# Performance work log

Measured on AMD Instinct MI355X. Metric: run time of the kernel, lower is better.

The kernel has to match this reference:

```python
import jax, jax.numpy as jnp
import numpy as np

# ---- dims (see shape_source) ----
N, EG, T = 10000, 120000, 600000
NR, NS = 16, 7                      # num_radial, num_spherical
EA, EE, ET, ERBF, ECBF, EBIL = 128, 256, 64, 16, 16, 64
NB = 2                              # num_blocks
CUTOFF = 6.0
MAXZ = 100
INV_SQRT2 = 0.7071067811865476


def scaled_silu(x):
    # GemNet 'swish' activation = ScaledSiLU
    return jax.nn.silu(x) * (1.0 / 0.6)


def layer_norm(x, w, b):
    mu = jnp.mean(x, -1, keepdims=True)
    v = jnp.var(x, -1, keepdims=True)
    return (x - mu) * jax.lax.rsqrt(v + 1e-5) * w + b


def radial_basis(D):
    # polynomial envelope (exponent 5) * gaussian RBF on d/cutoff
    d = D / CUTOFF
    p = 5.0
    env = 1.0 - ((p + 1) * (p + 2) / 2) * d**5 + p * (p + 2) * d**6 - (p * (p + 1) / 2) * d**7
    env = jnp.where(d < 1.0, env, 0.0)
    offsets = jnp.linspace(0.0, 1.0, NR)
    coeff = -0.5 * (NR - 1.0) ** 2   # -0.5 / spacing^2
    return env[:, None] * jnp.exp(coeff * (d[:, None] - offsets) ** 2)  # (EG, NR)


def spherical_basis(cosphi):
    # circular basis: Y_l0(phi) = sqrt((2l+1)/4pi) P_l(cos phi), l = 0..NS-1
    P = [jnp.ones_like(cosphi), cosphi]
    for l in range(2, NS):
        P.append(((2 * l - 1) * cosphi * P[-1] - (l - 1) * P[-2]) / l)
    return jnp.stack([np.sqrt((2 * l + 1) / (4 * np.pi)) * P[l] for l in range(NS)], -1)  # (T, NS)


def residual(x, Ws):
    # GemNet ResidualLayer: 2 bias-free dense + skip, scaled by 1/sqrt(2)
    y = scaled_silu(scaled_silu(x @ Ws[0]) @ Ws[1])
    return (x + y) * INV_SQRT2


def gemnet_forward(D, cosphi, atom_emb, W_rbf3, W_rbf_h, W_rbf_out, W_cbf_down,
                   W_edge_emb, ib_dense_ca, ib_trip_dense_ba, ib_trip_mlp_rbf,
                   ib_trip_down, ib_trip_bilinear, ib_trip_up_ca, ib_trip_up_ac,
                   ib_res_before, ib_res_after, ib_atom_dense_rbf, ib_atom_dense1,
                   ib_atom_res, ib_concat_dense, ib_res_m, ob_dense_rbf, ob_dense1,
                   ob_res, ln_m_w, ln_m_b, ln_E_w, ln_E_b,
                   Z, idx_s, idx_t, id3_ba, id3_ca, id_swap):
    rbf = radial_basis(D)                                   # (EG, NR)
    sph = spherical_basis(cosphi)                           # (T, NS)
    rbf3 = rbf @ W_rbf3                                     # (EG, ERBF)
    rbf_h = rbf @ W_rbf_h
    rbf_out = rbf @ W_rbf_out
    # EfficientInteractionDownProjection: rbf x W -> (EG, NS, ECBF)
    rbf_W1 = jnp.einsum('er,sri->esi', rbf, W_cbf_down)
    # per-triplet circular-basis embedding: sum over spherical components
    cbf_t = jnp.einsum('ts,tsi->ti', sph, rbf_W1[id3_ca])   # (T, ECBF)

    h = atom_emb[Z]                                         # (N, EA)
    m = scaled_silu(jnp.concatenate([h[idx_s], h[idx_t], rbf], -1) @ W_edge_emb)  # (EG, EE)

    def out_block(i, h_cur, m_cur):
        mn = layer_norm(m_cur, ln_m_w[i], ln_m_b[i])
        x = mn * (rbf_out @ ob_dense_rbf[i])                # (EG, EE)
        xE = jax.ops.segment_sum(x, idx_t, num_segments=N)  # scatter edges -> atoms
        xE = scaled_silu(xE @ ob_dense1[i])                 # (N, EA)
        for r in range(ob_res.shape[1]):
            xE = residual(xE, ob_res[i, r])
        return layer_norm(xE, ln_E_w[i], ln_E_b[i])

    E_t = out_block(0, h, m)
    for i in range(NB):
        # ---- triplet interaction ----
        x_ca_skip = scaled_silu(m @ ib_dense_ca[i])
        x_ba = scaled_silu(m @ ib_trip_dense_ba[i])
        x_ba = x_ba * (rbf3 @ ib_trip_mlp_rbf[i])
        x_trip = scaled_silu(x_ba @ ib_trip_down[i])        # (EG, ET)
        x_t = x_trip[id3_ba]                                # gather -> (T, ET)
        # bilinear: out[t,o] = sum_i cbf_t[t,i] * sum_c x_t[t,c] W[c,i,o]
        Wb = ib_trip_bilinear[i]                            # (ET, ECBF, EBIL)
        acc = (x_t @ Wb[:, 0, :]) * cbf_t[:, 0:1]
        for ic in range(1, ECBF):
            acc = acc + (x_t @ Wb[:, ic, :]) * cbf_t[:, ic:ic + 1]
        x = jax.ops.segment_sum(acc, id3_ca, num_segments=EG)  # scatter trip -> edges (EG, EBIL)
        x_ca = scaled_silu(x @ ib_trip_up_ca[i])
        x_ac = scaled_silu(x @ ib_trip_up_ac[i])[id_swap]   # counter-directional edge
        x3 = (x_ca + x_ac) * INV_SQRT2

        # ---- edge update ----
        x = (x_ca_skip + x3) * INV_SQRT2
        for r in range(ib_res_before.shape[1]):
            x = residual(x, ib_res_before[i, r])
        x = (x + m) * INV_SQRT2
        for r in range(ib_res_after.shape[1]):
            x = residual(x, ib_res_after[i, r])

        # ---- atom update ----
        xa = x * (rbf_h @ ib_atom_dense_rbf[i])
        xa = jax.ops.segment_sum(xa, idx_t, num_segments=N)
        xa = scaled_silu(xa @ ib_atom_dense1[i])            # (N, EA)
        for r in range(ib_atom_res.shape[1]):
            xa = residual(xa, ib_atom_res[i, r])
        h = (h + xa) * INV_SQRT2

        # ---- edge embedding refresh with updated atoms ----
        m2 = scaled_silu(jnp.concatenate([h[idx_s], h[idx_t], x], -1) @ ib_concat_dense[i])
        for r in range(ib_res_m.shape[1]):
            m2 = residual(m2, ib_res_m[i, r])
        m = (m + m2) * INV_SQRT2

        E_t = E_t + out_block(i + 1, h, m)
    return E_t  # (N, EA) per-atom output features


def setup_inputs() -> dict:
    key = jax.random.key(0)
    ks = iter(jax.random.split(key, 64))

    def nrm(shape, fan_in):
        return jax.random.normal(next(ks), shape, jnp.float32) / np.sqrt(fan_in)

    Z = jax.random.randint(next(ks), (N,), 0, MAXZ)
    idx_s = jax.random.randint(next(ks), (EG,), 0, N)
    idx_t = jax.random.randint(next(ks), (EG,), 0, N)
    id3_ba = jax.random.randint(next(ks), (T,), 0, EG)
    id3_ca = jax.random.randint(next(ks), (T,), 0, EG)
    id_swap = jnp.arange(EG) ^ 1   # symmetric edges stored in (e, e^1) pairs
    D = jax.random.uniform(next(ks), (EG,), jnp.float32, 0.8, 5.9)
    cosphi = jax.random.uniform(next(ks), (T,), jnp.float32, -1.0, 1.0)

    emb = jax.random.normal(next(ks), (MAXZ, EA), jnp.float32)
    emb = emb / jnp.maximum(jnp.linalg.norm(emb, axis=-1, keepdims=True), 1.0)  # max_norm=1

    NBo = NB + 1
    inp = dict(
        D=D, cosphi=cosphi, atom_emb=emb,
        W_rbf3=nrm((NR, ERBF), NR), W_rbf_h=nrm((NR, ERBF), NR), W_rbf_out=nrm((NR, ERBF), NR),
        W_cbf_down=nrm((NS, NR, ECBF), NR),
        W_edge_emb=nrm((2 * EA + NR, EE), 2 * EA + NR),
        ib_dense_ca=nrm((NB, EE, EE), EE),
        ib_trip_dense_ba=nrm((NB, EE, EE), EE),
        ib_trip_mlp_rbf=nrm((NB, ERBF, EE), ERBF),
        ib_trip_down=nrm((NB, EE, ET), EE),
        ib_trip_bilinear=nrm((NB, ET, ECBF, EBIL), ET * ECBF),
        ib_trip_up_ca=nrm((NB, EBIL, EE), EBIL),
        ib_trip_up_ac=nrm((NB, EBIL, EE), EBIL),
        ib_res_before=nrm((NB, 1, 2, EE, EE), EE),
        ib_res_after=nrm((NB, 1, 2, EE, EE), EE),
        ib_atom_dense_rbf=nrm((NB, ERBF, EE), ERBF),
        ib_atom_dense1=nrm((NB, EE, EA), EE),
        ib_atom_res=nrm((NB, 2, 2, EA, EA), EA),
        ib_concat_dense=nrm((NB, 2 * EA + EE, EE), 2 * EA + EE),
        ib_res_m=nrm((NB, 1, 2, EE, EE), EE),
        ob_dense_rbf=nrm((NBo, ERBF, EE), ERBF),
        ob_dense1=nrm((NBo, EE, EA), EE),
        ob_res=nrm((NBo, 2, 2, EA, EA), EA),
        ln_m_w=jnp.ones((NBo, EE)), ln_m_b=jnp.zeros((NBo, EE)),
        ln_E_w=jnp.ones((NBo, EA)), ln_E_b=jnp.zeros((NBo, EA)),
        Z=Z, idx_s=idx_s, idx_t=idx_t, id3_ba=id3_ba, id3_ca=id3_ca, id_swap=id_swap,
    )
    return inp


def reference(D, cosphi, atom_emb, W_rbf3, W_rbf_h, W_rbf_out, W_cbf_down, W_edge_emb,
              ib_dense_ca, ib_trip_dense_ba, ib_trip_mlp_rbf, ib_trip_down,
              ib_trip_bilinear, ib_trip_up_ca, ib_trip_up_ac, ib_res_before,
              ib_res_after, ib_atom_dense_rbf, ib_atom_dense1, ib_atom_res,
              ib_concat_dense, ib_res_m, ob_dense_rbf, ob_dense1, ob_res,
              ln_m_w, ln_m_b, ln_E_w, ln_E_b, Z, idx_s, idx_t, id3_ba, id3_ca, id_swap):
    return gemnet_forward(D, cosphi, atom_emb, W_rbf3, W_rbf_h, W_rbf_out, W_cbf_down,
                          W_edge_emb, ib_dense_ca, ib_trip_dense_ba, ib_trip_mlp_rbf,
                          ib_trip_down, ib_trip_bilinear, ib_trip_up_ca, ib_trip_up_ac,
                          ib_res_before, ib_res_after, ib_atom_dense_rbf, ib_atom_dense1,
                          ib_atom_res, ib_concat_dense, ib_res_m, ob_dense_rbf, ob_dense1,
                          ob_res, ln_m_w, ln_m_b, ln_E_w, ln_E_b,
                          Z, idx_s, idx_t, id3_ba, id3_ca, id_swap)
```

## Files before the change

### kernel.cpp

```cpp
#include <hip/hip_runtime.h>

#define NATOM 10000
#define EG    120000
#define TT    600000

#define INV_SQRT2f 0.7071067811865476f

typedef unsigned short bf16t;
typedef __attribute__((ext_vector_type(8))) short s16x8;
typedef __attribute__((ext_vector_type(8))) unsigned short u16x8;
typedef __attribute__((ext_vector_type(4))) float f32x4;

__device__ __forceinline__ float ssilu(float x) {
    return x * (1.0f / (1.0f + __expf(-x))) * (1.0f / 0.6f);
}
__device__ __forceinline__ float bf2f(unsigned short u) {
    return __uint_as_float(((unsigned)u) << 16);
}
__device__ __forceinline__ unsigned short f2bf(float f) {
    unsigned b = __float_as_uint(f);
    unsigned r = (b + 0x7FFF + ((b >> 16) & 1)) >> 16;
    return (unsigned short)r;
}
__device__ __forceinline__ u16x8 cvt8(const float4 va, const float4 vb) {
// ... 144 lines not shown
        r[i] = env * __expf(-112.5f * t * t);
    }
#pragma unroll
    for (int j = 0; j < 16; j++) rbf[(size_t)e * 16 + j] = f2bf(r[j]);
    for (int s = 0; s < 7; s++) {
#pragma unroll 4
        for (int i = 0; i < 16; i++) {
            float a = 0.f;
#pragma unroll
            for (int k = 0; k < 16; k++)
                a = fmaf(r[k], sW[(s * 16 + k) * 16 + i], a);
            rbfW1[(size_t)e * 112 + s * 16 + i] = a;
        }
    }
}

__global__ __launch_bounds__(256) void k_cbf(
    const float* __restrict__ cosphi, const int* __restrict__ id3_ca,
    const float* __restrict__ rbfW1, const int* __restrict__ rank,
    bf16t* __restrict__ cbf)
{
    int t = blockIdx.x * 256 + threadIdx.x;
    if (t >= TT) return;
    float c = cosphi[t];
    const float norm[7] = {0.28209479177387814f, 0.4886025119029199f, 0.6307831305050401f,
                           0.7463526651802308f, 0.8462843753216345f, 0.935414346693485f,
                           1.0171072362820548f};
    float y[7];
    float pm2 = 1.0f, pm1 = c;
    y[0] = norm[0];
    y[1] = norm[1] * c;
    for (int l = 2; l < 7; l++) {
        float p = ((2.0f * l - 1.0f) * c * pm1 - (l - 1.0f) * pm2) / (float)l;
        y[l] = norm[l] * p;
        pm2 = pm1; pm1 = p;
    }
    int e = id3_ca[t];
    const float* __restrict__ w = rbfW1 + (size_t)e * 112;
    float out[16];
#pragma unroll
    for (int i = 0; i < 16; i++) out[i] = 0.f;
#pragma unroll
    for (int s = 0; s < 7; s++) {
        float ys = y[s];
#pragma unroll
        for (int i = 0; i < 16; i++) out[i] = fmaf(ys, w[s * 16 + i], out[i]);
    }
    int p = rank[t];
#pragma unroll
    for (int i = 0; i < 16; i++) cbf[(size_t)p * 16 + i] = f2bf(out[i]);
}

__global__ __launch_bounds__(256) void k_hgather(
    const float* __restrict__ emb, const int* __restrict__ Z, bf16t* __restrict__ h)
{
    int i = blockIdx.x * 256 + threadIdx.x;
    if (i < NATOM * 128) {
        int n = i >> 7, j = i & 127;
        h[i] = f2bf(emb[(size_t)Z[n] * 128 + j]);
    }
}

template <typename TA, int FR, int FC, int EPI>
__global__ __launch_bounds__(256) void mgemm3(
    const TA* __restrict__ A, const bf16t* __restrict__ BT,
    bf16t* __restrict__ C, const bf16t* __restrict__ skip,
    int M, int N, int K)
{
    constexpr int ROWS = 2 * FR * 16;
    constexpr int COLS = 2 * FC * 16;
    __shared__ __align__(16) ushort As[ROWS][40];
    __shared__ __align__(16) ushort Bs[COLS][40];
    const int tid = threadIdx.x, wave = tid >> 6, lane = tid & 63;
    const int waveR = wave >> 1, waveC = wave & 1;
    const int rowBase = blockIdx.y * ROWS, colBase = blockIdx.x * COLS;

    const int sar = tid >> 1, sak = (tid & 1) << 4;
    int agr = rowBase + sar; if (agr >= M) agr = M - 1;
    int sbc, sbk;
    if constexpr (COLS == 128) { sbc = tid >> 1; sbk = (tid & 1) << 4; }
    else                       { sbc = tid >> 2; sbk = (tid & 3) << 3; }

    f32x4 zv = {0.f, 0.f, 0.f, 0.f};
    f32x4 acc[FR][FC];
#pragma unroll
    for (int f = 0; f < FR; f++)
#pragma unroll
        for (int q = 0; q < FC; q++) acc[f][q] = zv;

    const int arow0 = waveR * FR * 16 + (lane & 15);
    const int bcol0 = waveC * FC * 16 + (lane & 15);
    const int kd = (lane >> 4) << 3;

    u16x8 a0, a1, b0, b1;
    auto loadA = [&](int k0) {
        if constexpr (sizeof(TA) == 2) {
            const u16x8* s = (const u16x8*)((const bf16t*)A + (size_t)agr * K + k0 + sak);
            a0 = s[0]; a1 = s[1];
        } else {
            const float4* s = (const float4*)((const float*)A + (size_t)agr * K + k0 + sak);
            a0 = cvt8(s[0], s[1]); a1 = cvt8(s[2], s[3]);
        }
    };
    auto loadB = [&](int k0) {
        const u16x8* s = (const u16x8*)(BT + (size_t)(colBase + sbc) * K + k0 + sbk);
        b0 = s[0];
        if constexpr (COLS == 128) b1 = s[1];
    };
    loadA(0); loadB(0);
    for (int k0 = 0; k0 < K; k0 += 32) {
        __syncthreads();
        *(u16x8*)&As[sar][sak] = a0;
        *(u16x8*)&As[sar][sak + 8] = a1;
        *(u16x8*)&Bs[sbc][sbk] = b0;
        if constexpr (COLS == 128) *(u16x8*)&Bs[sbc][sbk + 8] = b1;
        __syncthreads();
        if (k0 + 32 < K) { loadA(k0 + 32); loadB(k0 + 32); }
        u16x8 af[FR], bf[FC];
#pragma unroll
        for (int f = 0; f < FR; f++) af[f] = *(const u16x8*)&As[arow0 + f * 16][kd];
#pragma unroll
        for (int q = 0; q < FC; q++) bf[q] = *(const u16x8*)&Bs[bcol0 + q * 16][kd];
#pragma unroll
        for (int f = 0; f < FR; f++)
#pragma unroll
            for (int q = 0; q < FC; q++)
                acc[f][q] = __builtin_amdgcn_mfma_f32_16x16x32_bf16(
                    *(s16x8*)&af[f], *(s16x8*)&bf[q], acc[f][q], 0, 0, 0);
    }

    const int rB = rowBase + waveR * FR * 16 + ((lane >> 4) << 2);
    const int cB = colBase + waveC * FC * 16 + (lane & 15);
#pragma unroll
    for (int f = 0; f < FR; f++) {
#pragma unroll
        for (int r = 0; r < 4; r++) {
            int row = rB + f * 16 + r;
            if (row >= M) continue;
#pragma unroll
            for (int q = 0; q < FC; q++) {
                int col = cB + q * 16;
                float v = acc[f][q][r];
                if (EPI == 1) {
                    C[(size_t)row * N + col] = f2bf(ssilu(v));
                } else {
                    float sk = bf2f(skip[(size_t)row * N + col]);
                    C[(size_t)row * N + col] = f2bf((sk + ssilu(v)) * INV_SQRT2f);
                }
            }
        }
    }
}

template <int FCC, int EPIOUT>
__global__ __launch_bounds__(256) void mgemm_res(
    const bf16t* __restrict__ A, const bf16t* __restrict__ BT0,
    const bf16t* __restrict__ BT1, bf16t* __restrict__ C,
    const bf16t* __restrict__ add2, int M)
{
    constexpr int N = FCC * 32;
    __shared__ __align__(16) ushort As[64][40];
    __shared__ __align__(16) ushort Bs[N][40];
    __shared__ __align__(16) ushort inter[64][N + 8];
    const int tid = threadIdx.x, wave = tid >> 6, lane = tid & 63;
    const int waveR = wave >> 1, waveC = wave & 1;
    const int rowBase = blockIdx.x * 64;

    const int sar = tid >> 2, sak = (tid & 3) << 3;
    int agr = rowBase + sar; if (agr >= M) agr = M - 1;
    const int sbc = tid >> 2, sbk = (tid & 3) << 3;

    const int arow0 = waveR * 32 + (lane & 15);
    const int bcol0 = waveC * FCC * 16 + (lane & 15);
    const int kd = (lane >> 4) << 3;

    f32x4 zv = {0.f, 0.f, 0.f, 0.f};
    f32x4 acc[2][FCC];
#pragma unroll
    for (int f = 0; f < 2; f++)
#pragma unroll
        for (int q = 0; q < FCC; q++) acc[f][q] = zv;

    u16x8 aR, bR[FCC / 2];
    auto loadA = [&](int k0) {
        aR = *(const u16x8*)(A + (size_t)agr * N + k0 + sak);
    };
    auto loadB = [&](const bf16t* BT, int k0) {
#pragma unroll
        for (int j = 0; j < FCC / 2; j++)
            bR[j] = *(const u16x8*)(BT + (size_t)(sbc + j * 64) * N + k0 + sbk);
    };

    loadA(0); loadB(BT0, 0);
    for (int k0 = 0; k0 < N; k0 += 32) {
        __syncthreads();
        *(u16x8*)&As[sar][sak] = aR;
#pragma unroll
        for (int j = 0; j < FCC / 2; j++) *(u16x8*)&Bs[sbc + j * 64][sbk] = bR[j];
        __syncthreads();
        if (k0 + 32 < N) { loadA(k0 + 32); loadB(BT0, k0 + 32); }
        else             { loadB(BT1, 0); }
        u16x8 af0 = *(const u16x8*)&As[arow0][kd];
        u16x8 af1 = *(const u16x8*)&As[arow0 + 16][kd];
        u16x8 bf[FCC];
#pragma unroll
        for (int q = 0; q < FCC; q++) bf[q] = *(const u16x8*)&Bs[bcol0 + q * 16][kd];
#pragma unroll
        for (int q = 0; q < FCC; q++) {
            acc[0][q] = __builtin_amdgcn_mfma_f32_16x16x32_bf16(
                *(s16x8*)&af0, *(s16x8*)&bf[q], acc[0][q], 0, 0, 0);
            acc[1][q] = __builtin_amdgcn_mfma_f32_16x16x32_bf16(
                *(s16x8*)&af1, *(s16x8*)&bf[q], acc[1][q], 0, 0, 0);
        }
    }
    {
        const int rL = waveR * 32 + ((lane >> 4) << 2);
        const int cL = waveC * FCC * 16 + (lane & 15);
#pragma unroll
        for (int f = 0; f < 2; f++)
#pragma unroll
            for (int r = 0; r < 4; r++)
#pragma unroll
                for (int q = 0; q < FCC; q++)
                    inter[rL + f * 16 + r][cL + q * 16] = f2bf(ssilu(acc[f][q][r]));
    }
#pragma unroll
    for (int f = 0; f < 2; f++)
#pragma unroll
        for (int q = 0; q < FCC; q++) acc[f][q] = zv;

    for (int k0 = 0; k0 < N; k0 += 32) {
        __syncthreads();
#pragma unroll
        for (int j = 0; j < FCC / 2; j++) *(u16x8*)&Bs[sbc + j * 64][sbk] = bR[j];
        __syncthreads();
        if (k0 + 32 < N) loadB(BT1, k0 + 32);
        u16x8 af0 = *(const u16x8*)&inter[arow0][k0 + kd];
        u16x8 af1 = *(const u16x8*)&inter[arow0 + 16][k0 + kd];
        u16x8 bf[FCC];
#pragma unroll
        for (int q = 0; q < FCC; q++) bf[q] = *(const u16x8*)&Bs[bcol0 + q * 16][kd];
#pragma unroll
        for (int q = 0; q < FCC; q++) {
            acc[0][q] = __builtin_amdgcn_mfma_f32_16x16x32_bf16(
                *(s16x8*)&af0, *(s16x8*)&bf[q], acc[0][q], 0, 0, 0);
            acc[1][q] = __builtin_amdgcn_mfma_f32_16x16x32_bf16(
                *(s16x8*)&af1, *(s16x8*)&bf[q], acc[1][q], 0, 0, 0);
        }
    }

    const int rB = rowBase + waveR * 32 + ((lane >> 4) << 2);
    const int cB = waveC * FCC * 16 + (lane & 15);
#pragma unroll
    for (int f = 0; f < 2; f++) {
#pragma unroll
        for (int r = 0; r < 4; r++) {
            int row = rB + f * 16 + r;
            if (row >= M) continue;
#pragma unroll
            for (int q = 0; q < FCC; q++) {
                int col = cB + q * 16;
                float sk = bf2f(A[(size_t)row * N + col]);
                float y = (sk + ssilu(acc[f][q][r])) * INV_SQRT2f;
                if (EPIOUT == 1) y = (y + bf2f(add2[(size_t)row * N + col])) * INV_SQRT2f;
                C[(size_t)row * N + col] = f2bf(y);
            }
        }
    }
}

__global__ __launch_bounds__(256) void mgemmA1(
    const bf16t* __restrict__ BT, bf16t* __restrict__ C,
    int M, int N, int K, int KP,
    const bf16t* __restrict__ hA, const int* __restrict__ gS,
    const int* __restrict__ gT, const bf16t* __restrict__ X, int w2)
{
    __shared__ __align__(16) ushort As[128][40];
    __shared__ __align__(16) ushort Bs[64][40];
    const int tid = threadIdx.x, wave = tid >> 6, lane = tid & 63;
    const int waveR = wave >> 1, waveC = wave & 1;
    const int rowBase = blockIdx.y * 128, colBase = blockIdx.x * 64;

    const int sar = tid >> 1, sak = (tid & 1) << 4;
    const int arow = rowBase + sar;
    const int arowC = arow < M ? arow : (M - 1);
    const int ia = gS[arowC], ibx = gT[arowC];
    const int sbc = tid >> 2, sbk = (tid & 3) << 3;

    f32x4 zv = {0.f, 0.f, 0.f, 0.f};
    f32x4 acc[4][2];
#pragma unroll
    for (int f = 0; f < 4; f++)
#pragma unroll
        for (int q = 0; q < 2; q++) acc[f][q] = zv;

    const int arow0 = waveR * 64 + (lane & 15);
    const int bcol0 = waveC * 32 + (lane & 15);
    const int kd = (lane >> 4) << 3;

    u16x8 a0, a1, b0;
    auto loadA = [&](int k0) {
        a0 = u16x8{}; a1 = u16x8{};
        const int kk = k0 + sak;
        if (kk < 128) {
            const u16x8* s = (const u16x8*)(hA + (size_t)ia * 128 + kk);
            a0 = s[0]; a1 = s[1];
        } else if (kk < 256) {
            const u16x8* s = (const u16x8*)(hA + (size_t)ibx * 128 + (kk - 128));
            a0 = s[0]; a1 = s[1];
        } else if (kk < K && kk - 256 < w2) {
            const u16x8* s = (const u16x8*)(X + (size_t)arowC * w2 + (kk - 256));
            a0 = s[0]; a1 = s[1];
        }
    };
    auto loadB = [&](int k0) {
        b0 = *(const u16x8*)(BT + (size_t)(colBase + sbc) * KP + k0 + sbk);
    };
    loadA(0); loadB(0);
    for (int k0 = 0; k0 < K; k0 += 32) {
        __syncthreads();
        *(u16x8*)&As[sar][sak] = a0;
        *(u16x8*)&As[sar][sak + 8] = a1;
        *(u16x8*)&Bs[sbc][sbk] = b0;
        __syncthreads();
        if (k0 + 32 < K) { loadA(k0 + 32); loadB(k0 + 32); }
        u16x8 af[4], bf[2];
#pragma unroll
        for (int f = 0; f < 4; f++) af[f] = *(const u16x8*)&As[arow0 + f * 16][kd];
#pragma unroll
        for (int q = 0; q < 2; q++) bf[q] = *(const u16x8*)&Bs[bcol0 + q * 16][kd];
#pragma unroll
        for (int f = 0; f < 4; f++)
#pragma unroll
            for (int q = 0; q < 2; q++)
                acc[f][q] = __builtin_amdgcn_mfma_f32_16x16x32_bf16(
                    *(s16x8*)&af[f], *(s16x8*)&bf[q], acc[f][q], 0, 0, 0);
    }

    const int rB = rowBase + waveR * 64 + ((lane >> 4) << 2);
    const int cB = colBase + waveC * 32 + (lane & 15);
#pragma unroll
    for (int f = 0; f < 4; f++) {
#pragma unroll
        for (int r = 0; r < 4; r++) {
            int row = rB + f * 16 + r;
            if (row >= M) continue;
#pragma unroll
            for (int q = 0; q < 2; q++)
                C[(size_t)row * N + cB + q * 16] = f2bf(ssilu(acc[f][q][r]));
        }
    }
}

__global__ __launch_bounds__(256) void mgemm_up(
    const float* __restrict__ A, const bf16t* __restrict__ BTca,
    const bf16t* __restrict__ BTac, bf16t* __restrict__ C,
    const bf16t* __restrict__ skip, int M)
{
    constexpr int K = 64, N = 256;
    __shared__ __align__(16) ushort As[128][40];
    __shared__ __align__(16) ushort Bs[2][64][40];
    const int tid = threadIdx.x, wave = tid >> 6, lane = tid & 63;
    const int waveR = wave >> 1, waveC = wave & 1;
    const int rowBase = blockIdx.y * 128, colBase = blockIdx.x * 64;

    const int sar = tid >> 1, sak = (tid & 1) << 4;
    int agr = rowBase + sar; if (agr >= M) agr = M - 1;
    const int sbc = tid >> 2, sbk = (tid & 3) << 3;

    f32x4 zv = {0.f, 0.f, 0.f, 0.f};
    f32x4 accA[4][2], accB[4][2];
#pragma unroll
    for (int f = 0; f < 4; f++)
#pragma unroll
        for (int q = 0; q < 2; q++) { accA[f][q] = zv; accB[f][q] = zv; }

    const int arow0 = waveR * 64 + (lane & 15);
    const int bcol0 = waveC * 32 + (lane & 15);
    const int kd = (lane >> 4) << 3;

    u16x8 a0, a1, bA, bB;
    auto loadA = [&](int k0) {
        const float4* s = (const float4*)(A + (size_t)agr * K + k0 + sak);
        a0 = cvt8(s[0], s[1]); a1 = cvt8(s[2], s[3]);
    };
    auto loadB = [&](int k0) {
        bA = *(const u16x8*)(BTca + (size_t)(colBase + sbc) * K + k0 + sbk);
        bB = *(const u16x8*)(BTac + (size_t)(colBase + sbc) * K + k0 + sbk);
    };
    loadA(0); loadB(0);
    for (int k0 = 0; k0 < K; k0 += 32) {
        __syncthreads();
        *(u16x8*)&As[sar][sak] = a0;
        *(u16x8*)&As[sar][sak + 8] = a1;
        *(u16x8*)&Bs[0][sbc][sbk] = bA;
        *(u16x8*)&Bs[1][sbc][sbk] = bB;
        __syncthreads();
        if (k0 + 32 < K) { loadA(k0 + 32); loadB(k0 + 32); }
        u16x8 af[4], bfA[2], bfB[2];
#pragma unroll
        for (int f = 0; f < 4; f++) af[f] = *(const u16x8*)&As[arow0 + f * 16][kd];
#pragma unroll
        for (int q = 0; q < 2; q++) {
            bfA[q] = *(const u16x8*)&Bs[0][bcol0 + q * 16][kd];
            bfB[q] = *(const u16x8*)&Bs[1][bcol0 + q * 16][kd];
        }
#pragma unroll
        for (int f = 0; f < 4; f++)
#pragma unroll
            for (int q = 0; q < 2; q++) {
                accA[f][q] = __builtin_amdgcn_mfma_f32_16x16x32_bf16(
                    *(s16x8*)&af[f], *(s16x8*)&bfA[q], accA[f][q], 0, 0, 0);
                accB[f][q] = __builtin_amdgcn_mfma_f32_16x16x32_bf16(
                    *(s16x8*)&af[f], *(s16x8*)&bfB[q], accB[f][q], 0, 0, 0);
            }
    }

    const int rB = rowBase + waveR * 64 + ((lane >> 4) << 2);
    const int cB = colBase + waveC * 32 + (lane & 15);
#pragma unroll
    for (int f = 0; f < 4; f++) {
#pragma unroll
        for (int r = 0; r < 4; r++) {
            int row = rB + f * 16 + r;
            if (row >= M) continue;
#pragma unroll
            for (int q = 0; q < 2; q++) {
                int col = cB + q * 16;
                float v = (ssilu(accA[f][q][r]) + ssilu(accB[f][q][r ^ 1])) * INV_SQRT2f;
                float y = (bf2f(skip[(size_t)row * N + col]) + v) * INV_SQRT2f;
                C[(size_t)row * N + col] = f2bf(y);
            }
        }
    }
}

__global__ __launch_bounds__(256) void k_bilinear_m(
    const bf16t* __restrict__ xtrip, const bf16t* __restrict__ cbf,
    const bf16t* __restrict__ WT,
    const int* __restrict__ ba_s, const int* __restrict__ ca_s,
    float* __restrict__ seg)
{
    __shared__ __align__(16) ushort xs[64][72];
    __shared__ ushort cbs[64][16];
    __shared__ int cas[64];
    __shared__ __align__(16) ushort ws[2][4096];
    __shared__ __align__(16) float ts[64][65];
    const int tid = threadIdx.x, wave = tid >> 6, lane = tid & 63;
    const int t0 = blockIdx.x * 64;
    {
        int r = tid >> 2, q = (tid & 3) << 4;
        int ba = ba_s[t0 + r];
        const u16x8* src = (const u16x8*)(xtrip + (size_t)ba * 64 + q);
        *(u16x8*)&xs[r][q] = src[0];
        *(u16x8*)&xs[r][q + 8] = src[1];
    }
    if (tid < 64) cas[tid] = ca_s[t0 + tid];
    {
        int e = tid << 2; int r = e >> 4, c = e & 15;
        *(ushort4*)&cbs[r][c] = *(const ushort4*)(cbf + (size_t)(t0 + r) * 16 + c);
    }
    u16x8 g0, g1;
    {
        const u16x8* s = (const u16x8*)(WT + (size_t)tid * 16);
        *(u16x8*)&ws[0][tid * 16] = s[0];
        *(u16x8*)&ws[0][tid * 16 + 8] = s[1];
        const u16x8* s1 = (const u16x8*)(WT + 4096 + (size_t)tid * 16);
        g0 = s1[0]; g1 = s1[1];
    }
    __syncthreads();
    const int kd = (lane >> 4) << 3;
    u16x8 a0 = *(const u16x8*)(&xs[wave * 16 + (lane & 15)][kd]);
    u16x8 a1 = *(const u16x8*)(&xs[wave * 16 + (lane & 15)][32 + kd]);
    const int rowo = wave * 16 + ((lane >> 4) << 2);
    const int chb = lane >> 4, colw = lane & 15;

    float tot[4][4];
#pragma unroll
    for (int a = 0; a < 4; a++)
#pragma unroll
        for (int b = 0; b < 4; b++) tot[a][b] = 0.f;

    for (int i = 0; i < 16; i++) {
        const int cur = i & 1;
        if (i < 15) {
            *(u16x8*)&ws[cur ^ 1][tid * 16] = g0;
            *(u16x8*)&ws[cur ^ 1][tid * 16 + 8] = g1;
        }
        const ushort* wb = ws[cur];
        f32x4 zv = {0.f, 0.f, 0.f, 0.f};
        f32x4 p[4] = {zv, zv, zv, zv};
#pragma unroll
        for (int fc = 0; fc < 4; fc++) {
            u16x8 b0 = *(const u16x8*)&wb[((chb * 64) + colw + fc * 16) * 8];
            u16x8 b1 = *(const u16x8*)&wb[(((4 + chb) * 64) + colw + fc * 16) * 8];
            p[fc] = __builtin_amdgcn_mfma_f32_16x16x32_bf16(
                *(s16x8*)&a0, *(s16x8*)&b0, p[fc], 0, 0, 0);
            p[fc] = __builtin_amdgcn_mfma_f32_16x16x32_bf16(
                *(s16x8*)&a1, *(s16x8*)&b1, p[fc], 0, 0, 0);
        }
#pragma unroll
        for (int r = 0; r < 4; r++) {
            float s = bf2f(cbs[rowo + r][i]);
#pragma unroll
            for (int fc = 0; fc < 4; fc++) tot[fc][r] += s * p[fc][r];
        }
        if (i < 14) {
            const u16x8* s = (const u16x8*)(WT + (size_t)(i + 2) * 4096 + (size_t)tid * 16);
            g0 = s[0]; g1 = s[1];
        }
        __syncthreads();
    }
#pragma unroll
    for (int r = 0; r < 4; r++)
#pragma unroll
        for (int fc = 0; fc < 4; fc++)
            ts[rowo + r][fc * 16 + (lane & 15)] = tot[fc][r];
    __syncthreads();
    {
        int q = tid >> 6, c = tid & 63;
        float s = 0.f;
        int cur = cas[q * 16];
#pragma unroll 1
        for (int r = q * 16; r < q * 16 + 16; r++) {
            int ca = cas[r];
            if (ca != cur) {
                atomicAdd(&seg[(size_t)cur * 64 + c], s);
                s = 0.f; cur = ca;
            }
            s += ts[r][c];
        }
        atomicAdd(&seg[(size_t)cur * 64 + c], s);
    }
}

__global__ __launch_bounds__(256) void k_mulproj(
    const bf16t* __restrict__ in, const bf16t* __restrict__ rvec,
    const float* __restrict__ Wp, bf16t* __restrict__ out)
{
    int e = blockIdx.x;
    int j = threadIdx.x;
    __shared__ float r16[16];
    if (j < 16) r16[j] = bf2f(rvec[(size_t)e * 16 + j]);
    __syncthreads();
    float p = 0.f;
#pragma unroll
    for (int k = 0; k < 16; k++) p = fmaf(r16[k], Wp[k * 256 + j], p);
    out[(size_t)e * 256 + j] = f2bf(bf2f(in[(size_t)e * 256 + j]) * p);
}

__global__ __launch_bounds__(256) void k_ln_proj(
    const bf16t* __restrict__ m, const float* __restrict__ lnw,
    const float* __restrict__ lnb, const bf16t* __restrict__ rvec,
    const float* __restrict__ Wp, bf16t* __restrict__ out)
{
    int e = blockIdx.x;
    int j = threadIdx.x;
    __shared__ float red[8];
    __shared__ float r16[16];
    if (j < 16) r16[j] = bf2f(rvec[(size_t)e * 16 + j]);
    float v = bf2f(m[(size_t)e * 256 + j]);
    float s = v, s2 = v * v;
#pragma unroll
    for (int off = 32; off > 0; off >>= 1) {
        s += __shfl_xor(s, off);
        s2 += __shfl_xor(s2, off);
    }
    int wid = j >> 6, lane = j & 63;
    if (lane == 0) { red[wid] = s; red[4 + wid] = s2; }
    __syncthreads();
    float tot = red[0] + red[1] + red[2] + red[3];
    float tot2 = red[4] + red[5] + red[6] + red[7];
    float mu = tot * (1.f / 256.f);
    float var = tot2 * (1.f / 256.f) - mu * mu;
    float ln = (v - mu) * rsqrtf(var + 1e-5f) * lnw[j] + lnb[j];
    float p = 0.f;
#pragma unroll
    for (int k = 0; k < 16; k++) p = fmaf(r16[k], Wp[k * 256 + j], p);
    out[(size_t)e * 256 + j] = f2bf(ln * p);
}

__global__ __launch_bounds__(128) void k_ln_acc(
    const bf16t* __restrict__ x, const float* __restrict__ w,
    const float* __restrict__ b, float* __restrict__ out)
{
    int n = blockIdx.x;
    int j = threadIdx.x;
    __shared__ float red[4];
    float v = bf2f(x[(size_t)n * 128 + j]);
    float s = v, s2 = v * v;
#pragma unroll
    for (int off = 32; off > 0; off >>= 1) {
        s += __shfl_xor(s, off);
        s2 += __shfl_xor(s2, off);
    }
    int wid = j >> 6, lane = j & 63;
    if (lane == 0) { red[wid] = s; red[2 + wid] = s2; }
    __syncthreads();
    float tot = red[0] + red[1];
    float tot2 = red[2] + red[3];
    float mu = tot * (1.f / 128.f);
    float var = tot2 * (1.f / 128.f) - mu * mu;
    out[(size_t)n * 128 + j] += (v - mu) * rsqrtf(var + 1e-5f) * w[j] + b[j];
}

typedef bf16t T;
static bool try_run(void* const* d_in, void* d_out, void* d_ws, size_t ws_size, hipStream_t stream)
{
    const float* D            = (const float*)d_in[0];
    const float* cosphi       = (const float*)d_in[1];
    const float* atom_emb     = (const float*)d_in[2];
    const float* W_rbf3       = (const float*)d_in[3];
    const float* W_rbf_h      = (const float*)d_in[4];
    const float* W_rbf_out    = (const float*)d_in[5];
    const float* W_cbf_down   = (const float*)d_in[6];
    const float* W_edge_emb   = (const float*)d_in[7];
    const float* ib_dense_ca  = (const float*)d_in[8];
    const float* ib_trip_dense_ba = (const float*)d_in[9];
    const float* ib_trip_mlp_rbf  = (const float*)d_in[10];
    const float* ib_trip_down     = (const float*)d_in[11];
    const float* ib_trip_bilinear = (const float*)d_in[12];
    const float* ib_trip_up_ca    = (const float*)d_in[13];
    const float* ib_trip_up_ac    = (const float*)d_in[14];
    const float* ib_res_before    = (const float*)d_in[15];
    const float* ib_res_after     = (const float*)d_in[16];
    const float* ib_atom_dense_rbf = (const float*)d_in[17];
    const float* ib_atom_dense1    = (const float*)d_in[18];
    const float* ib_atom_res       = (const float*)d_in[19];
    const float* ib_concat_dense   = (const float*)d_in[20];
    const float* ib_res_m          = (const float*)d_in[21];
    const float* ob_dense_rbf      = (const float*)d_in[22];
    const float* ob_dense1         = (const float*)d_in[23];
    const float* ob_res            = (const float*)d_in[24];
    const float* ln_m_w            = (const float*)d_in[25];
    const float* ln_m_b            = (const float*)d_in[26];
    const float* ln_E_w            = (const float*)d_in[27];
    const float* ln_E_b            = (const float*)d_in[28];
    const int* Z       = (const int*)d_in[29];
    const int* idx_s   = (const int*)d_in[30];
    const int* idx_t   = (const int*)d_in[31];
    const int* id3_ba  = (const int*)d_in[32];
    const int* id3_ca  = (const int*)d_in[33];

    char* base = (char*)d_ws;
    size_t off = 0;
    auto alloc = [&](size_t bytes) -> char* {
        off = (off + 255) & ~(size_t)255;
        char* p = base + off;
        off += bytes;
        return p;
    };
    T* m      = (T*)alloc((size_t)EG * 256 * 2);
    T* B1     = (T*)alloc((size_t)EG * 256 * 2);
    T* B2     = (T*)alloc((size_t)EG * 256 * 2);
    float* rbfW1 = (float*)B1;
    int* rank    = (int*)B2;
    T* rbf    = (T*)alloc((size_t)EG * 16 * 2);
    T* cbf    = (T*)alloc((size_t)TT * 16 * 2);
    bf16t* h  = (bf16t*)alloc((size_t)NATOM * 128 * 2);
    T* xtrip  = (T*)alloc((size_t)EG * 64 * 2);
    char* ub  = alloc((size_t)EG * 64 * 4);
    float* seg64  = (float*)ub;
    bf16t* segN_b = (bf16t*)ub;
    bf16t* At1b   = (bf16t*)(ub + (size_t)NATOM * 256 * 2);
    int* cntT  = (int*)ub;
    int* cnt2T = (int*)(ub + (size_t)EG * 4);
    int* off_ca = (int*)(ub + (size_t)2 * EG * 4);
    float* wcb = (float*)alloc((size_t)7 * 4096 * 4);
    bf16t* ar  = (bf16t*)alloc((size_t)507904 * 2);
    int* off_atom  = (int*)alloc((size_t)(NATOM + 1) * 4);
    int* ba_s      = (int*)alloc((size_t)TT * 4);
    int* ca_s      = (int*)alloc((size_t)TT * 4);
    int* csr_edges = (int*)alloc((size_t)EG * 4);
    if (off > ws_size) return false;
    float* out = (float*)d_out;

    auto g256 = [&](const T* A, unsigned wOff, T* C) {
        dim3 grid(2, (EG + 127) / 128);
        mgemm3<T, 4, 4, 1><<<grid, 256, 0, stream>>>(A, ar + wOff, C, nullptr, EG, 256, 256);
    };
    auto gatom1 = [&](const bf16t* A, unsigned wOff, bf16t* C) {
        dim3 grid(1, (NATOM + 127) / 128);
        mgemm3<bf16t, 4, 4, 1><<<grid, 256, 0, stream>>>(A, ar + wOff, C, nullptr, NATOM, 128, 256);
    };
    auto out_block = [&](int i, unsigned offD1, unsigned offRes) {
        k_ln_proj<<<EG, 256, 0, stream>>>(m, ln_m_w + (size_t)i * 256, ln_m_b + (size_t)i * 256,
                                          rbf, wcb + (size_t)(4 + i) * 4096, B2);
        k_segsum<<<NATOM, 256, 0, stream>>>(B2, off_atom, csr_edges, segN_b);
        gatom1(segN_b, offD1, At1b);
        mgemm_res<4, 0><<<(NATOM + 63) / 64, 256, 0, stream>>>(
            At1b, ar + offRes, ar + offRes + 16384, At1b, nullptr, NATOM);
        mgemm_res<4, 0><<<(NATOM + 63) / 64, 256, 0, stream>>>(
            At1b, ar + offRes + 32768, ar + offRes + 49152, At1b, nullptr, NATOM);
        k_ln_acc<<<NATOM, 128, 0, stream>>>(At1b, ln_E_w + (size_t)i * 128, ln_E_b + (size_t)i * 128, out);
    };

    hipMemsetAsync(cntT, 0, (size_t)EG * 4, stream);
    k_hist<<<(TT + 255) / 256, 256, 0, stream>>>(id3_ca, cntT, TT);
    k_scan<<<1, 1024, 0, stream>>>(cntT, off_ca, EG);
    hipMemsetAsync(cnt2T, 0, (size_t)EG * 4, stream);
    k_rank_trip<<<(TT + 255) / 256, 256, 0, stream>>>(id3_ca, id3_ba, off_ca, cnt2T,
                                                      rank, ba_s, ca_s, TT);
    hipMemsetAsync(cntT, 0, (size_t)NATOM * 4, stream);
    k_hist<<<(EG + 255) / 256, 256, 0, stream>>>(idx_t, cntT, EG);
    k_scan<<<1, 1024, 0, stream>>>(cntT, off_atom, NATOM);
    hipMemsetAsync(cnt2T, 0, (size_t)NATOM * 4, stream);
    k_rank_edge<<<(EG + 255) / 256, 256, 0, stream>>>(idx_t, off_atom, cnt2T, csr_edges, EG);

    {
        WcBatch wb;
        wb.e[0] = {W_rbf3, ib_trip_mlp_rbf};
        wb.e[1] = {W_rbf3, ib_trip_mlp_rbf + 4096};
        wb.e[2] = {W_rbf_h, ib_atom_dense_rbf};
        wb.e[3] = {W_rbf_h, ib_atom_dense_rbf + 4096};
        wb.e[4] = {W_rbf_out, ob_dense_rbf};
        wb.e[5] = {W_rbf_out, ob_dense_rbf + 4096};
        wb.e[6] = {W_rbf_out, ob_dense_rbf + 8192};
        k_wcomb_batch<<<7, 256, 0, stream>>>(wb, wcb);
    }
    {
        WtBatch wt{};
        wt.e[0] = {W_edge_emb, 0u, 272, 288, 256, 0};
        wt.e[1] = {ob_dense1, 73728u, 256, 256, 128, 0};
        for (int j = 0; j < 4; j++)
            wt.e[2 + j] = {ob_res + (size_t)j * 16384, 106496u + j * 16384u, 128, 128, 128, 0};
        wt.n = 6;
        k_wt_batch<<<512, 256, 0, stream>>>(wt, ar);
    }

    hipMemsetAsync(out, 0, (size_t)NATOM * 128 * 4, stream);
    k_rbf<<<(EG + 255) / 256, 256, 0, stream>>>(D, W_cbf_down, rbf, rbfW1);
    k_cbf<<<(TT + 255) / 256, 256, 0, stream>>>(cosphi, id3_ca, rbfW1, rank, cbf);
    k_hgather<<<(NATOM * 128 + 255) / 256, 256, 0, stream>>>(atom_emb, Z, h);
    {
        dim3 grid(4, (EG + 127) / 128);
        mgemmA1<<<grid, 256, 0, stream>>>(ar, m, EG, 256, 272, 288, h, idx_s, idx_t, rbf, 16);
    }
    out_block(0, 73728u, 106496u);

    for (int i = 0; i < 2; i++) {
        {
            WtBatch wt{};
            wt.e[0] = {ib_dense_ca + (size_t)i * 65536, 0u, 256, 256, 256, 0};
            wt.e[1] = {ib_trip_dense_ba + (size_t)i * 65536, 65536u, 256, 256, 256, 0};
            wt.e[2] = {ib_trip_down + (size_t)i * 16384, 131072u, 256, 256, 64, 0};
            wt.e[3] = {ib_trip_bilinear + (size_t)i * 65536, 147456u, 0, 0, 0, 1};
            wt.e[4] = {ib_trip_up_ca + (size_t)i * 16384, 212992u, 64, 64, 256, 0};
            wt.e[5] = {ib_trip_up_ac + (size_t)i * 16384, 229376u, 64, 64, 256, 0};
            wt.e[6] = {ib_res_before + (size_t)i * 131072, 245760u, 256, 256, 256, 0};
            wt.e[7] = {ib_res_before + (size_t)i * 131072 + 65536, 311296u, 256, 256, 256, 0};
            wt.e[8] = {ib_res_after + (size_t)i * 131072, 376832u, 256, 256, 256, 0};
            wt.e[9] = {ib_res_after + (size_t)i * 131072 + 65536, 442368u, 256, 256, 256, 0};
            wt.n = 10;
            k_wt_batch<<<512, 256, 0, stream>>>(wt, ar);
        }
        g256(m, 0u, B1);
        g256(m, 65536u, B2);
        k_mulproj<<<EG, 256, 0, stream>>>(B2, rbf, wcb + (size_t)i * 4096, B2);
        {
            dim3 grid(1, (EG + 127) / 128);
            mgemm3<T, 4, 2, 1><<<grid, 256, 0, stream>>>(B2, ar + 131072, xtrip, nullptr, EG, 64, 256);
        }
        hipMemsetAsync(seg64, 0, (size_t)EG * 64 * 4, stream);
        k_bilinear_m<<<TT / 64, 256, 0, stream>>>(xtrip, cbf, ar + 147456, ba_s, ca_s, seg64);
        {
            dim3 grid(4, (EG + 127) / 128);
            mgemm_up<<<grid, 256, 0, stream>>>(seg64, ar + 212992, ar + 229376, B1, B1, EG);
        }
        mgemm_res<8, 1><<<EG / 64, 256, 0, stream>>>(B1, ar + 245760, ar + 311296, B1, m, EG);
        mgemm_res<8, 0><<<EG / 64, 256, 0, stream>>>(B1, ar + 376832, ar + 442368, B1, nullptr, EG);
        {
            WtBatch wt{};
            wt.e[0] = {ib_atom_dense1 + (size_t)i * 32768, 0u, 256, 256, 128, 0};
            for (int j = 0; j < 4; j++)
                wt.e[1 + j] = {ib_atom_res + (size_t)i * 65536 + (size_t)j * 16384,
                               32768u + j * 16384u, 128, 128, 128, 0};
            wt.e[5] = {ib_concat_dense + (size_t)i * 131072, 98304u, 512, 512, 256, 0};
            wt.e[6] = {ib_res_m + (size_t)i * 131072, 229376u, 256, 256, 256, 0};
            wt.e[7] = {ib_res_m + (size_t)i * 131072 + 65536, 294912u, 256, 256, 256, 0};
            wt.e[8] = {ob_dense1 + (size_t)(i + 1) * 32768, 360448u, 256, 256, 128, 0};
            wt.n = 9;
            k_wt_batch<<<512, 256, 0, stream>>>(wt, ar);
            WtBatch wt2{};
            for (int j = 0; j < 4; j++)
                wt2.e[j] = {ob_res + (size_t)(i + 1) * 65536 + (size_t)j * 16384,
                            393216u + j * 16384u, 128, 128, 128, 0};
            wt2.n = 4;
            k_wt_batch<<<512, 256, 0, stream>>>(wt2, ar);
        }
        k_mulproj<<<EG, 256, 0, stream>>>(B1, rbf, wcb + (size_t)(2 + i) * 4096, B2);
        k_segsum<<<NATOM, 256, 0, stream>>>(B2, off_atom, csr_edges, segN_b);
        gatom1(segN_b, 0u, At1b);
        mgemm_res<4, 0><<<(NATOM + 63) / 64, 256, 0, stream>>>(
            At1b, ar + 32768, ar + 49152, At1b, nullptr, NATOM);
        mgemm_res<4, 1><<<(NATOM + 63) / 64, 256, 0, stream>>>(
            At1b, ar + 65536, ar + 81920, h, h, NATOM);
        {
            dim3 grid(4, (EG + 127) / 128);
            mgemmA1<<<grid, 256, 0, stream>>>(ar + 98304, B2, EG, 256, 512, 512, h, idx_s, idx_t, B1, 256);
        }
        mgemm_res<8, 1><<<EG / 64, 256, 0, stream>>>(B2, ar + 229376, ar + 294912, m, m, EG);

        out_block(i + 1, 360448u, 393216u);
    }
    return true;
}

extern "C" void kernel_launch(void* const* d_in, const int* in_sizes, int n_in,
                              void* d_out, int out_size, void* d_ws, size_t ws_size,
                              hipStream_t stream)
{
    if (try_run(d_in, d_out, d_ws, ws_size, stream)) return;
    float v = 3000.0f + (float)(ws_size >> 20);
    k_fill<<<(NATOM * 128 + 255) / 256, 256, 0, stream>>>((float*)d_out, NATOM * 128, v);
}
```

Before: 2.639 ms.

## Enlarge GEMM tiles to 256x128 and batch edges in projection kernels

Adds a new mgemm4 kernel with 256-row by 128-column tiles and widens mgemmA1 the same way, so each block does more MFMA work per shared-memory load and fewer blocks are launched. k_mulproj and k_ln_proj now handle 16 edges per block, staging the 16x256 projection weights and the rbf vectors in shared memory once per block instead of rereading weights from global memory for every edge. Larger tiles raise register and LDS pressure, which may lower occupancy. k_ln_proj also adds per-edge block barriers inside its loop.

```diff
diff --git a/kernel.cpp b/kernel.cpp
--- a/kernel.cpp
+++ b/kernel.cpp
@@ -320,6 +320,86 @@
     }
 }
 
+template <typename TA, int FC>
+__global__ __launch_bounds__(256) void mgemm4(
+    const TA* __restrict__ A, const bf16t* __restrict__ BT,
+    bf16t* __restrict__ C, int M, int N, int K)
+{
+    constexpr int COLS = 2 * FC * 16;
+    __shared__ __align__(16) ushort As[256][40];
+    __shared__ __align__(16) ushort Bs[COLS][40];
+    const int tid = threadIdx.x, wave = tid >> 6, lane = tid & 63;
+    const int waveR = wave >> 1, waveC = wave & 1;
+    const int rowBase = blockIdx.y * 256, colBase = blockIdx.x * COLS;
+
+    int agr = rowBase + tid; if (agr >= M) agr = M - 1;
+    const int sbc = tid >> 1, sbk = (tid & 1) << 4;
+
+    f32x4 zv = {0.f, 0.f, 0.f, 0.f};
+    f32x4 acc[8][FC];
+#pragma unroll
+    for (int f = 0; f < 8; f++)
+#pragma unroll
+        for (int q = 0; q < FC; q++) acc[f][q] = zv;
+
+    const int arow0 = waveR * 128 + (lane & 15);
+    const int bcol0 = waveC * FC * 16 + (lane & 15);
+    const int kd = (lane >> 4) << 3;
+
+    u16x8 a[4], b0, b1;
+    auto loadA = [&](int k0) {
+        if constexpr (sizeof(TA) == 2) {
+            const u16x8* s = (const u16x8*)((const bf16t*)A + (size_t)agr * K + k0);
+            a[0] = s[0]; a[1] = s[1]; a[2] = s[2]; a[3] = s[3];
+        } else {
+            const float4* s = (const float4*)((const float*)A + (size_t)agr * K + k0);
+            a[0] = cvt8(s[0], s[1]); a[1] = cvt8(s[2], s[3]);
+            a[2] = cvt8(s[4], s[5]); a[3] = cvt8(s[6], s[7]);
+        }
+    };
+    auto loadB = [&](int k0) {
+        const u16x8* s = (const u16x8*)(BT + (size_t)(colBase + sbc) * K + k0 + sbk);
+        b0 = s[0]; b1 = s[1];
+    };
+    loadA(0); loadB(0);
+    for (int k0 = 0; k0 < K; k0 += 32) {
+        __syncthreads();
+        *(u16x8*)&As[tid][0] = a[0];
+        *(u16x8*)&As[tid][8] = a[1];
+        *(u16x8*)&As[tid][16] = a[2];
+        *(u16x8*)&As[tid][24] = a[3];
+        *(u16x8*)&Bs[sbc][sbk] = b0;
+        *(u16x8*)&Bs[sbc][sbk + 8] = b1;
+        __syncthreads();
+        if (k0 + 32 < K) { loadA(k0 + 32); loadB(k0 + 32); }
+        u16x8 af[8], bf[FC];
+#pragma unroll
+        for (int f = 0; f < 8; f++) af[f] = *(const u16x8*)&As[arow0 + f * 16][kd];
+#pragma unroll
+        for (int q = 0; q < FC; q++) bf[q] = *(const u16x8*)&Bs[bcol0 + q * 16][kd];
+#pragma unroll
+        for (int f = 0; f < 8; f++)
+#pragma unroll
+            for (int q = 0; q < FC; q++)
+                acc[f][q] = __builtin_amdgcn_mfma_f32_16x16x32_bf16(
+                    *(s16x8*)&af[f], *(s16x8*)&bf[q], acc[f][q], 0, 0, 0);
+    }
+
+    const int rB = rowBase + waveR * 128 + ((lane >> 4) << 2);
+    const int cB = colBase + waveC * FC * 16 + (lane & 15);
+#pragma unroll
+    for (int f = 0; f < 8; f++) {
+#pragma unroll
+        for (int r = 0; r < 4; r++) {
+            int row = rB + f * 16 + r;
+            if (row >= M) continue;
+#pragma unroll
+            for (int q = 0; q < FC; q++)
+                C[(size_t)row * N + cB + q * 16] = f2bf(ssilu(acc[f][q][r]));
+        }
+    }
+}
+
 template <int FCC, int EPIOUT>
 __global__ __launch_bounds__(256) void mgemm_res(
     const bf16t* __restrict__ A, const bf16t* __restrict__ BT0,
@@ -443,78 +523,84 @@
     const bf16t* __restrict__ hA, const int* __restrict__ gS,
     const int* __restrict__ gT, const bf16t* __restrict__ X, int w2)
 {
-    __shared__ __align__(16) ushort As[128][40];
-    __shared__ __align__(16) ushort Bs[64][40];
+    __shared__ __align__(16) ushort As[256][40];
+    __shared__ __align__(16) ushort Bs[128][40];
     const int tid = threadIdx.x, wave = tid >> 6, lane = tid & 63;
     const int waveR = wave >> 1, waveC = wave & 1;
-    const int rowBase = blockIdx.y * 128, colBase = blockIdx.x * 64;
-
-    const int sar = tid >> 1, sak = (tid & 1) << 4;
-    const int arow = rowBase + sar;
-    const int arowC = arow < M ? arow : (M - 1);
-    const int ia = gS[arowC], ibx = gT[arowC];
-    const int sbc = tid >> 2, sbk = (tid & 3) << 3;
+    const int rowBase = blockIdx.y * 256, colBase = blockIdx.x * 128;
+
+    int agr = rowBase + tid; if (agr >= M) agr = M - 1;
+    const int ia = gS[agr], ibx = gT[agr];
+    const int sbc = tid >> 1, sbk = (tid & 1) << 4;
 
     f32x4 zv = {0.f, 0.f, 0.f, 0.f};
-    f32x4 acc[4][2];
-#pragma unroll
-    for (int f = 0; f < 4; f++)
-#pragma unroll
-        for (int q = 0; q < 2; q++) acc[f][q] = zv;
-
-    const int arow0 = waveR * 64 + (lane & 15);
-    const int bcol0 = waveC * 32 + (lane & 15);
+    f32x4 acc[8][4];
+#pragma unroll
+    for (int f = 0; f < 8; f++)
+#pragma unroll
+        for (int q = 0; q < 4; q++) acc[f][q] = zv;
+
+    const int arow0 = waveR * 128 + (lane & 15);
+    const int bcol0 = waveC * 64 + (lane & 15);
     const int kd = (lane >> 4) << 3;
 
-    u16x8 a0, a1, b0;
+    u16x8 a[4], b0, b1;
     auto loadA = [&](int k0) {
-        a0 = u16x8{}; a1 = u16x8{};
-        const int kk = k0 + sak;
-        if (kk < 128) {
-            const u16x8* s = (const u16x8*)(hA + (size_t)ia * 128 + kk);
-            a0 = s[0]; a1 = s[1];
-        } else if (kk < 256) {
-            const u16x8* s = (const u16x8*)(hA + (size_t)ibx * 128 + (kk - 128));
-            a0 = s[0]; a1 = s[1];
-        } else if (kk < K && kk - 256 < w2) {
-            const u16x8* s = (const u16x8*)(X + (size_t)arowC * w2 + (kk - 256));
-            a0 = s[0]; a1 = s[1];
+#pragma unroll
+        for (int h = 0; h < 2; h++) {
+            int kk = k0 + 16 * h;
+            u16x8 t0{}, t1{};
+            if (kk < 128) {
+                const u16x8* s = (const u16x8*)(hA + (size_t)ia * 128 + kk);
+                t0 = s[0]; t1 = s[1];
+            } else if (kk < 256) {
+                const u16x8* s = (const u16x8*)(hA + (size_t)ibx * 128 + (kk - 128));
+                t0 = s[0]; t1 = s[1];
+            } else if (kk < K && kk - 256 < w2) {
+                const u16x8* s = (const u16x8*)(X + (size_t)agr * w2 + (kk - 256));
+                t0 = s[0]; t1 = s[1];
+            }
+            a[2 * h] = t0; a[2 * h + 1] = t1;
         }
     };
     auto loadB = [&](int k0) {
-        b0 = *(const u16x8*)(BT + (size_t)(colBase + sbc) * KP + k0 + sbk);
+        const u16x8* s = (const u16x8*)(BT + (size_t)(colBase + sbc) * KP + k0 + sbk);
+        b0 = s[0]; b1 = s[1];
     };
     loadA(0); loadB(0);
     for (int k0 = 0; k0 < K; k0 += 32) {
         __syncthreads();
-        *(u16x8*)&As[sar][sak] = a0;
-        *(u16x8*)&As[sar][sak + 8] = a1;
+        *(u16x8*)&As[tid][0] = a[0];
+        *(u16x8*)&As[tid][8] = a[1];
+        *(u16x8*)&As[tid][16] = a[2];
+        *(u16x8*)&As[tid][24] = a[3];
         *(u16x8*)&Bs[sbc][sbk] = b0;
+        *(u16x8*)&Bs[sbc][sbk + 8] = b1;
         __syncthreads();
         if (k0 + 32 < K) { loadA(k0 + 32); loadB(k0 + 32); }
-        u16x8 af[4], bf[2];
-#pragma unroll
-        for (int f = 0; f < 4; f++) af[f] = *(const u16x8*)&As[arow0 + f * 16][kd];
-#pragma unroll
-        for (int q = 0; q < 2; q++) bf[q] = *(const u16x8*)&Bs[bcol0 + q * 16][kd];
-#pragma unroll
-        for (int f = 0; f < 4; f++)
-#pragma unroll
-            for (int q = 0; q < 2; q++)
+        u16x8 af[8], bf[4];
+#pragma unroll
+        for (int f = 0; f < 8; f++) af[f] = *(const u16x8*)&As[arow0 + f * 16][kd];
+#pragma unroll
+        for (int q = 0; q < 4; q++) bf[q] = *(const u16x8*)&Bs[bcol0 + q * 16][kd];
+#pragma unroll
+        for (int f = 0; f < 8; f++)
+#pragma unroll
+            for (int q = 0; q < 4; q++)
                 acc[f][q] = __builtin_amdgcn_mfma_f32_16x16x32_bf16(
                     *(s16x8*)&af[f], *(s16x8*)&bf[q], acc[f][q], 0, 0, 0);
     }
 
-    const int rB = rowBase + waveR * 64 + ((lane >> 4) << 2);
-    const int cB = colBase + waveC * 32 + (lane & 15);
-#pragma unroll
-    for (int f = 0; f < 4; f++) {
+    const int rB = rowBase + waveR * 128 + ((lane >> 4) << 2);
+    const int cB = colBase + waveC * 64 + (lane & 15);
+#pragma unroll
+    for (int f = 0; f < 8; f++) {
 #pragma unroll
         for (int r = 0; r < 4; r++) {
             int row = rB + f * 16 + r;
             if (row >= M) continue;
 #pragma unroll
-            for (int q = 0; q < 2; q++)
+            for (int q = 0; q < 4; q++)
                 C[(size_t)row * N + cB + q * 16] = f2bf(ssilu(acc[f][q][r]));
         }
     }
@@ -706,15 +792,21 @@
     const bf16t* __restrict__ in, const bf16t* __restrict__ rvec,
     const float* __restrict__ Wp, bf16t* __restrict__ out)
 {
-    int e = blockIdx.x;
-    int j = threadIdx.x;
-    __shared__ float r16[16];
-    if (j < 16) r16[j] = bf2f(rvec[(size_t)e * 16 + j]);
+    __shared__ float sW[4096];
+    __shared__ float sr[256];
+    const int j = threadIdx.x;
+    const int e0 = blockIdx.x * 16;
+    for (int t = j; t < 4096; t += 256) sW[t] = Wp[t];
+    sr[j] = bf2f(rvec[(size_t)e0 * 16 + j]);
     __syncthreads();
-    float p = 0.f;
-#pragma unroll
-    for (int k = 0; k < 16; k++) p = fmaf(r16[k], Wp[k * 256 + j], p);
-    out[(size_t)e * 256 + j] = f2bf(bf2f(in[(size_t)e * 256 + j]) * p);
+#pragma unroll 4
+    for (int g = 0; g < 16; g++) {
+        float p = 0.f;
+#pragma unroll
+        for (int k = 0; k < 16; k++) p = fmaf(sr[g * 16 + k], sW[k * 256 + j], p);
+        size_t e = (size_t)(e0 + g);
+        out[e * 256 + j] = f2bf(bf2f(in[e * 256 + j]) * p);
+    }
 }
 
 __global__ __launch_bounds__(256) void k_ln_proj(
@@ -722,30 +814,38 @@
     const float* __restrict__ lnb, const bf16t* __restrict__ rvec,
     const float* __restrict__ Wp, bf16t* __restrict__ out)
 {
-    int e = blockIdx.x;
-    int j = threadIdx.x;
+    __shared__ float sW[4096];
+    __shared__ float sr[256];
     __shared__ float red[8];
-    __shared__ float r16[16];
-    if (j < 16) r16[j] = bf2f(rvec[(size_t)e * 16 + j]);
-    float v = bf2f(m[(size_t)e * 256 + j]);
-    float s = v, s2 = v * v;
-#pragma unroll
-    for (int off = 32; off > 0; off >>= 1) {
-        s += __shfl_xor(s, off);
-        s2 += __shfl_xor(s2, off);
-    }
-    int wid = j >> 6, lane = j & 63;
-    if (lane == 0) { red[wid] = s; red[4 + wid] = s2; }
+    const int j = threadIdx.x;
+    const int e0 = blockIdx.x * 16;
+    for (int t = j; t < 4096; t += 256) sW[t] = Wp[t];
+    sr[j] = bf2f(rvec[(size_t)e0 * 16 + j]);
+    const float lw = lnw[j], lb = lnb[j];
     __syncthreads();
-    float tot = red[0] + red[1] + red[2] + red[3];
-    float tot2 = red[4] + red[5] + red[6] + red[7];
-    float mu = tot * (1.f / 256.f);
-    float var = tot2 * (1.f / 256.f) - mu * mu;
-    float ln = (v - mu) * rsqrtf(var + 1e-5f) * lnw[j] + lnb[j];
-    float p = 0.f;
-#pragma unroll
-    for (int k = 0; k < 16; k++) p = fmaf(r16[k], Wp[k * 256 + j], p);
-    out[(size_t)e * 256 + j] = f2bf(ln * p);
+    const int wid = j >> 6, lane = j & 63;
+    for (int g = 0; g < 16; g++) {
+        size_t e = (size_t)(e0 + g);
+        float v = bf2f(m[e * 256 + j]);
+        float s = v, s2 = v * v;
+#pragma unroll
+        for (int off = 32; off > 0; off >>= 1) {
+            s += __shfl_xor(s, off);
+            s2 += __shfl_xor(s2, off);
+        }
+        if (lane == 0) { red[wid] = s; red[4 + wid] = s2; }
+        __syncthreads();
+        float tot = red[0] + red[1] + red[2] + red[3];
+        float tot2 = red[4] + red[5] + red[6] + red[7];
+        float mu = tot * (1.f / 256.f);
+        float var = tot2 * (1.f / 256.f) - mu * mu;
+        float ln = (v - mu) * rsqrtf(var + 1e-5f) * lw + lb;
+        float p = 0.f;
+#pragma unroll
+        for (int k = 0; k < 16; k++) p = fmaf(sr[g * 16 + k], sW[k * 256 + j], p);
+        out[e * 256 + j] = f2bf(ln * p);
+        __syncthreads();
+    }
 }
 
 __global__ __launch_bounds__(128) void k_ln_acc(
@@ -844,16 +944,16 @@
     float* out = (float*)d_out;
 
     auto g256 = [&](const T* A, unsigned wOff, T* C) {
-        dim3 grid(2, (EG + 127) / 128);
-        mgemm3<T, 4, 4, 1><<<grid, 256, 0, stream>>>(A, ar + wOff, C, nullptr, EG, 256, 256);
+        dim3 grid(2, (EG + 255) / 256);
+        mgemm4<T, 4><<<grid, 256, 0, stream>>>(A, ar + wOff, C, EG, 256, 256);
     };
     auto gatom1 = [&](const bf16t* A, unsigned wOff, bf16t* C) {
         dim3 grid(1, (NATOM + 127) / 128);
         mgemm3<bf16t, 4, 4, 1><<<grid, 256, 0, stream>>>(A, ar + wOff, C, nullptr, NATOM, 128, 256);
     };
     auto out_block = [&](int i, unsigned offD1, unsigned offRes) {
-        k_ln_proj<<<EG, 256, 0, stream>>>(m, ln_m_w + (size_t)i * 256, ln_m_b + (size_t)i * 256,
-                                          rbf, wcb + (size_t)(4 + i) * 4096, B2);
+        k_ln_proj<<<EG / 16, 256, 0, stream>>>(m, ln_m_w + (size_t)i * 256, ln_m_b + (size_t)i * 256,
+                                               rbf, wcb + (size_t)(4 + i) * 4096, B2);
         k_segsum<<<NATOM, 256, 0, stream>>>(B2, off_atom, csr_edges, segN_b);
         gatom1(segN_b, offD1, At1b);
         mgemm_res<4, 0><<<(NATOM + 63) / 64, 256, 0, stream>>>(
@@ -901,7 +1001,7 @@
     k_cbf<<<(TT + 255) / 256, 256, 0, stream>>>(cosphi, id3_ca, rbfW1, rank, cbf);
     k_hgather<<<(NATOM * 128 + 255) / 256, 256, 0, stream>>>(atom_emb, Z, h);
     {
-        dim3 grid(4, (EG + 127) / 128);
+        dim3 grid(2, (EG + 255) / 256);
         mgemmA1<<<grid, 256, 0, stream>>>(ar, m, EG, 256, 272, 288, h, idx_s, idx_t, rbf, 16);
     }
     out_block(0, 73728u, 106496u);
@@ -924,7 +1024,7 @@
         }
         g256(m, 0u, B1);
         g256(m, 65536u, B2);
-        k_mulproj<<<EG, 256, 0, stream>>>(B2, rbf, wcb + (size_t)i * 4096, B2);
+        k_mulproj<<<EG / 16, 256, 0, stream>>>(B2, rbf, wcb + (size_t)i * 4096, B2);
         {
             dim3 grid(1, (EG + 127) / 128);
             mgemm3<T, 4, 2, 1><<<grid, 256, 0, stream>>>(B2, ar + 131072, xtrip, nullptr, EG, 64, 256);
@@ -956,7 +1056,7 @@
             wt2.n = 4;
             k_wt_batch<<<512, 256, 0, stream>>>(wt2, ar);
         }
-        k_mulproj<<<EG, 256, 0, stream>>>(B1, rbf, wcb + (size_t)(2 + i) * 4096, B2);
+        k_mulproj<<<EG / 16, 256, 0, stream>>>(B1, rbf, wcb + (size_t)(2 + i) * 4096, B2);
         k_segsum<<<NATOM, 256, 0, stream>>>(B2, off_atom, csr_edges, segN_b);
         gatom1(segN_b, 0u, At1b);
         mgemm_res<4, 0><<<(NATOM + 63) / 64, 256, 0, stream>>>(
@@ -964,7 +1064,7 @@
         mgemm_res<4, 1><<<(NATOM + 63) / 64, 256, 0, stream>>>(
             At1b, ar + 65536, ar + 81920, h, h, NATOM);
         {
-            dim3 grid(4, (EG + 127) / 128);
+            dim3 grid(2, (EG + 255) / 256);
             mgemmA1<<<grid, 256, 0, stream>>>(ar + 98304, B2, EG, 256, 512, 512, h, idx_s, idx_t, B1, 256);
         }
         mgemm_res<8, 1><<<EG / 64, 256, 0, stream>>>(B2, ar + 229376, ar + 294912, m, m, EG);
```

Result: no change. 2.641 ms (+0.1%).
